# Performance work log

Hardware: AMD Instinct MI355X
Metric: run time of the kernel (lower is better)

The kernel has to match this reference:

```python
import jax, jax.numpy as jnp
import numpy as np

D_MODEL = 1024
N_HEADS = 16
HEAD_DIM = D_MODEL // N_HEADS


def setup_inputs() -> dict:
    key = jax.random.key(0)
    k1, k2, k3 = jax.random.split(key, 3)
    x = jax.random.normal(k1, (4, 2048, D_MODEL), dtype=jnp.float32)
    # torch Linear(d, 3d, bias=False): y = x @ W.T ; store transposed weight [d, 3d]
    scale = 1.0 / np.sqrt(D_MODEL)
    W_qkv = jax.random.normal(k2, (D_MODEL, 3 * D_MODEL), dtype=jnp.float32) * scale
    W_proj = jax.random.normal(k3, (D_MODEL, D_MODEL), dtype=jnp.float32) * scale
    return {"x": x, "W_qkv": W_qkv, "W_proj": W_proj}


def reference(x, W_qkv, W_proj):
    B, T, C = x.shape
    h, d = N_HEADS, HEAD_DIM
    qkv = x @ W_qkv                      # [B,T,3C]
    q, k, v = jnp.split(qkv, 3, axis=-1)
    def split_heads(t):
        return t.reshape(B, T, h, d).transpose(0, 2, 1, 3)  # [B,h,T,d]
    q, k, v = map(split_heads, (q, k, v))
    att = jnp.einsum('bhqd,bhkd->bhqk', q, k) / np.sqrt(d)  # [B,h,T,T]
    causal = jnp.tril(jnp.ones((T, T), dtype=bool))
    att = jnp.where(causal, att, -jnp.inf)
    att = jax.nn.softmax(att, axis=-1)
    # dropout = 0.0 (eval mode): no-op
    y = jnp.einsum('bhqk,bhkd->bhqd', att, v)               # [B,h,T,d]
    y = y.transpose(0, 2, 1, 3).reshape(B, T, C)
    return y @ W_proj
```

## Files before the change

### kernel.cpp

```cpp
#include <hip/hip_runtime.h>

#define T_SEQ 2048
#define D_MODEL 1024
#define NB 4
#define NH 16
#define HD 64

typedef __attribute__((ext_vector_type(8))) __bf16 bf16x8;
typedef __attribute__((ext_vector_type(4))) __bf16 bf16x4;
typedef __attribute__((ext_vector_type(4))) float f32x4;

__device__ __forceinline__ void gload_lds16(const void* g, void* l) {
  __builtin_amdgcn_global_load_lds((const __attribute__((address_space(1))) unsigned int*)g,
                                   (__attribute__((address_space(3))) unsigned int*)l,
                                   16, 0, 0);
}

__device__ __forceinline__ unsigned int pack_bf16_2(float e0, float e1) {
  unsigned short u0 = __builtin_bit_cast(unsigned short, (__bf16)e0);
  unsigned short u1 = __builtin_bit_cast(unsigned short, (__bf16)e1);
  return (unsigned int)u0 | ((unsigned int)u1 << 16);
}

__global__ __launch_bounds__(256) void cvt_bf16_kernel(const float* __restrict__ s,
                                                       __bf16* __restrict__ d, int n) {
  int i = (blockIdx.x * 256 + threadIdx.x) * 8;
  if (i >= n) return;
  float4 a = *(const float4*)(s + i);
  float4 b = *(const float4*)(s + i + 4);
  bf16x8 v;
  v[0] = (__bf16)a.x; v[1] = (__bf16)a.y; v[2] = (__bf16)a.z; v[3] = (__bf16)a.w;
  v[4] = (__bf16)b.x; v[5] = (__bf16)b.y; v[6] = (__bf16)b.z; v[7] = (__bf16)b.w;
  *(bf16x8*)(d + i) = v;
}

__global__ __launch_bounds__(256) void transpose_cvt_kernel(const float* __restrict__ W,
                                                            __bf16* __restrict__ Wt,
                                                            int K, int N) {
  __shared__ float t[32][33];
  int tx = threadIdx.x, ty = threadIdx.y;
  int n0 = blockIdx.x * 32, k0 = blockIdx.y * 32;
#pragma unroll
  for (int r = 0; r < 4; ++r)
    t[ty + r * 8][tx] = W[(size_t)(k0 + ty + r * 8) * N + n0 + tx];
  __syncthreads();
#pragma unroll
  for (int r = 0; r < 4; ++r)
    Wt[(size_t)(n0 + ty + r * 8) * K + k0 + tx] = (__bf16)t[tx][ty + r * 8];
}

__global__ __launch_bounds__(256) void extract_vt_kernel(const __bf16* __restrict__ qkv,
                                                         __bf16* __restrict__ Vt) {
  __shared__ __bf16 t[32][34];
  int tx = threadIdx.x, ty = threadIdx.y;
  int tt = blockIdx.x * 32;
  int dt = blockIdx.y * 32;
  int bh = blockIdx.z;
  int b = bh >> 4, h = bh & 15;
#pragma unroll
  for (int r = 0; r < 4; ++r)
    t[ty + r * 8][tx] = qkv[(size_t)(b * T_SEQ + tt + ty + r * 8) * 3072 + 2048 + h * HD + dt + tx];
  __syncthreads();
#pragma unroll
  for (int r = 0; r < 4; ++r)
    Vt[(size_t)(bh * HD + dt + ty + r * 8) * T_SEQ + tt + tx] = t[tx][ty + r * 8];
}

template <typename OutT>
__global__ __launch_bounds__(256) void gemm_bt(const __bf16* __restrict__ A,
                                               const __bf16* __restrict__ Bt,
                                               OutT* __restrict__ C,
                                               int M, int N, int K) {
  __shared__ __bf16 lA[128 * 64];
  __shared__ __bf16 lB[128 * 64];
  int tid = threadIdx.x;
  int lane = tid & 63, w = tid >> 6;
  int wm = w >> 1, wn = w & 1;
  int nwgx = gridDim.x;
  int lid = blockIdx.y * nwgx + blockIdx.x;
  int cpx = (nwgx * gridDim.y) >> 3;
  int swz = (lid & 7) * cpx + (lid >> 3);
  int bn = swz % nwgx, bm = swz / nwgx;
  f32x4 acc[4][4] = {};
  for (int kt = 0; kt < K; kt += 64) {
#pragma unroll
    for (int it = 0; it < 4; ++it) {
      int o = it * 4096 + tid * 16;
      int row = o >> 7;
      int ss = ((o >> 4) & 7) ^ (row & 7);
      gload_lds16(A + (size_t)(bm * 128 + row) * K + kt + ss * 8, (char*)lA + o);
      gload_lds16(Bt + (size_t)(bn * 128 + row) * K + kt + ss * 8, (char*)lB + o);
    }
    __syncthreads();
    bf16x8 af[4][2], bfv[4][2];
#pragma unroll
    for (int i = 0; i < 4; ++i)
#pragma unroll
      for (int kk = 0; kk < 2; ++kk) {
        int ra = wm * 64 + i * 16 + (lane & 15);
        int sa = ((lane >> 4) + kk * 4) ^ (ra & 7);
        af[i][kk] = *(const bf16x8*)((const char*)lA + ra * 128 + sa * 16);
        int rb = wn * 64 + i * 16 + (lane & 15);
        int sb = ((lane >> 4) + kk * 4) ^ (rb & 7);
        bfv[i][kk] = *(const bf16x8*)((const char*)lB + rb * 128 + sb * 16);
      }
#pragma unroll
    for (int kk = 0; kk < 2; ++kk)
#pragma unroll
      for (int i = 0; i < 4; ++i)
#pragma unroll
        for (int j = 0; j < 4; ++j)
          acc[i][j] = __builtin_amdgcn_mfma_f32_16x16x32_bf16(af[i][kk], bfv[j][kk], acc[i][j], 0, 0, 0);
    __syncthreads();
  }
#pragma unroll
  for (int i = 0; i < 4; ++i)
#pragma unroll
    for (int j = 0; j < 4; ++j)
#pragma unroll
      for (int r = 0; r < 4; ++r) {
        int row = bm * 128 + wm * 64 + i * 16 + (lane >> 4) * 4 + r;
        int col = bn * 128 + wn * 64 + j * 16 + (lane & 15);
        C[(size_t)row * N + col] = (OutT)acc[i][j][r];
      }
}

__global__ __launch_bounds__(128) void attn_kernel(const __bf16* __restrict__ qkv,
                                                   const __bf16* __restrict__ Vt,
                                                   __bf16* __restrict__ Y) {
  __shared__ __bf16 lK[2][64 * 64];
  __shared__ __bf16 lV[2][64 * 64];
  int tid = threadIdx.x, lane = tid & 63, w = tid >> 6;
  int q = lane & 15, g = lane >> 4;

  int l = blockIdx.x;
  int pairHB = ((l & 7) << 3) | (l >> 7);
  int p = (l >> 3) & 15;
  int h = pairHB & 15, b = pairHB >> 4;

  const float SCALE = 0.125f * 1.44269504088896f;
  const f32x4 fzero = {0.f, 0.f, 0.f, 0.f};

#pragma unroll 1
  for (int pass = 0; pass < 2; ++pass) {
    int qt = pass ? p : 31 - p;

    bf16x8 qf[2][2];
#pragma unroll
    for (int qi = 0; qi < 2; ++qi) {
      const __bf16* qp =
          qkv + (size_t)(b * T_SEQ + qt * 64 + w * 32 + qi * 16 + q) * 3072 + h * HD;
      qf[qi][0] = *(const bf16x8*)(qp + g * 8);
      qf[qi][1] = *(const bf16x8*)(qp + 32 + g * 8);
#pragma unroll
      for (int kk = 0; kk < 2; ++kk)
#pragma unroll
        for (int jj = 0; jj < 8; ++jj)
          qf[qi][kk][jj] = (__bf16)((float)qf[qi][kk][jj] * SCALE);
    }

    float m[2] = {-INFINITY, -INFINITY}, lsum[2] = {0.f, 0.f};
    f32x4 yacc[2][4];
#pragma unroll
    for (int qi = 0; qi < 2; ++qi)
#pragma unroll
      for (int f = 0; f < 4; ++f) yacc[qi][f] = fzero;

    asm volatile("s_waitcnt vmcnt(0)" ::: "memory");
    __builtin_amdgcn_sched_barrier(0);

    auto STAGE = [&](int kvt, int bi) {
#pragma unroll
      for (int it = 0; it < 4; ++it) {
        int o = it * 2048 + tid * 16;
        int row = o >> 7;
        int ss = ((o >> 4) & 7) ^ (row & 7);
        gload_lds16(qkv + (size_t)(b * T_SEQ + kvt * 64 + row) * 3072 + 1024 + h * HD + ss * 8,
                    (char*)lK[bi] + o);
        gload_lds16(Vt + (size_t)((b * NH + h) * HD + row) * T_SEQ + kvt * 64 + ss * 8,
                    (char*)lV[bi] + o);
      }
    };

    STAGE(0, 0);

#pragma unroll 1
    for (int kvt = 0; kvt <= qt; ++kvt) {
      int cur = kvt & 1;
      if (kvt < qt) {
        STAGE(kvt + 1, cur ^ 1);
        asm volatile("s_waitcnt vmcnt(8)" ::: "memory");
      } else {
        asm volatile("s_waitcnt vmcnt(0)" ::: "memory");
      }
      __builtin_amdgcn_sched_barrier(0);
      __builtin_amdgcn_s_barrier();
      __builtin_amdgcn_sched_barrier(0);

      f32x4 s[2][4];
#pragma unroll
      for (int qi = 0; qi < 2; ++qi)
#pragma unroll
        for (int f = 0; f < 4; ++f) s[qi][f] = fzero;
      const char* Kbase = (const char*)lK[cur];
      __builtin_amdgcn_s_setprio(1);
#pragma unroll
      for (int kk = 0; kk < 2; ++kk)
#pragma unroll
        for (int f = 0; f < 4; ++f) {
          int rk = f * 16 + q;
          int sk = (g + kk * 4) ^ (rk & 7);
          bf16x8 kf = *(const bf16x8*)(Kbase + rk * 128 + sk * 16);
#pragma unroll
          for (int qi = 0; qi < 2; ++qi)
            s[qi][f] = __builtin_amdgcn_mfma_f32_16x16x32_bf16(kf, qf[qi][kk], s[qi][f], 0, 0, 0);
        }
      __builtin_amdgcn_s_setprio(0);

      if (kvt == qt) {
#pragma unroll
        for (int qi = 0; qi < 2; ++qi) {
          int qloc = w * 32 + qi * 16 + q;
#pragma unroll
          for (int f = 0; f < 4; ++f)
#pragma unroll
            for (int r = 0; r < 4; ++r)
              if (f * 16 + g * 4 + r > qloc) s[qi][f][r] = -INFINITY;
        }
      }

      float mx[2];
#pragma unroll
      for (int qi = 0; qi < 2; ++qi) {
        float v = fmaxf(fmaxf(fmaxf(s[qi][0][0], s[qi][0][1]), fmaxf(s[qi][0][2], s[qi][0][3])),
                        fmaxf(fmaxf(s[qi][1][0], s[qi][1][1]), fmaxf(s[qi][1][2], s[qi][1][3])));
        v = fmaxf(v, fmaxf(fmaxf(fmaxf(s[qi][2][0], s[qi][2][1]), fmaxf(s[qi][2][2], s[qi][2][3])),
                           fmaxf(fmaxf(s[qi][3][0], s[qi][3][1]), fmaxf(s[qi][3][2], s[qi][3][3]))));
        v = fmaxf(v, __shfl_xor(v, 16, 64));
        v = fmaxf(v, __shfl_xor(v, 32, 64));
        mx[qi] = v;
      }

      float growth = fmaxf(mx[0] - m[0], mx[1] - m[1]);
      if (__any(growth > 8.0f)) {
#pragma unroll
        for (int qi = 0; qi < 2; ++qi) {
          float mn = fmaxf(m[qi], mx[qi]);
          float al = exp2f(m[qi] - mn);
          m[qi] = mn;
          lsum[qi] *= al;
#pragma unroll
          for (int r = 0; r < 4; ++r) {
            float ar = __shfl(al, g * 4 + r, 64);
#pragma unroll
            for (int f = 0; f < 4; ++f) yacc[qi][f][r] *= ar;
          }
        }
      }

      unsigned int Wd[2][4][2];
#pragma unroll
      for (int qi = 0; qi < 2; ++qi) {
        float ps = 0.f;
#pragma unroll
        for (int f = 0; f < 4; ++f)
#pragma unroll
          for (int hh = 0; hh < 2; ++hh) {
            float e0 = exp2f(s[qi][f][2 * hh] - m[qi]);
            float e1 = exp2f(s[qi][f][2 * hh + 1] - m[qi]);
            ps += e0 + e1;
            Wd[qi][f][hh] = pack_bf16_2(e0, e1);
          }
        lsum[qi] += ps;
      }

      int srcA = ((g & 1) << 5) | q;
      int srcB = srcA + 16;
      bool hisel = (g >= 2);
      bf16x8 pa[2][2];
#pragma unroll
      for (int qi = 0; qi < 2; ++qi)
#pragma unroll
        for (int kk = 0; kk < 2; ++kk) {
          unsigned int pw[4];
#pragma unroll
          for (int t = 0; t < 4; ++t) {
            int src = (t < 2) ? srcA : srcB;
            unsigned int c0 = (unsigned int)__shfl((int)Wd[qi][2 * kk][t & 1], src, 64);
            unsigned int c1 = (unsigned int)__shfl((int)Wd[qi][2 * kk + 1][t & 1], src, 64);
            pw[t] = hisel ? c1 : c0;
          }
          uint4 u = make_uint4(pw[0], pw[1], pw[2], pw[3]);
          pa[qi][kk] = __builtin_bit_cast(bf16x8, u);
        }

      const char* Vbase = (const char*)lV[cur];
      __builtin_amdgcn_s_setprio(1);
#pragma unroll
      for (int kk = 0; kk < 2; ++kk)
#pragma unroll
        for (int f = 0; f < 4; ++f) {
          int rv = f * 16 + q;
          int sv2 = (g + kk * 4) ^ (rv & 7);
          bf16x8 vf = *(const bf16x8*)(Vbase + rv * 128 + sv2 * 16);
#pragma unroll
          for (int qi = 0; qi < 2; ++qi)
            yacc[qi][f] = __builtin_amdgcn_mfma_f32_16x16x32_bf16(pa[qi][kk], vf, yacc[qi][f], 0, 0, 0);
        }
      __builtin_amdgcn_s_setprio(0);

      __builtin_amdgcn_sched_barrier(0);
      asm volatile("s_waitcnt lgkmcnt(0)" ::: "memory");
      __builtin_amdgcn_s_barrier();
      __builtin_amdgcn_sched_barrier(0);
    }

#pragma unroll
    for (int qi = 0; qi < 2; ++qi) {
      float ls = lsum[qi];
      ls += __shfl_xor(ls, 16, 64);
      ls += __shfl_xor(ls, 32, 64);
      float linv = 1.0f / ls;
      int qrow = qt * 64 + w * 32 + qi * 16 + g * 4;
#pragma unroll
      for (int r = 0; r < 4; ++r) {
        float lr = __shfl(linv, g * 4 + r, 64);
#pragma unroll
        for (int f = 0; f < 4; ++f) {
          Y[(size_t)(b * T_SEQ + qrow + r) * D_MODEL + h * HD + f * 16 + q] =
              (__bf16)(yacc[qi][f][r] * lr);
        }
      }
    }
  }
}

extern "C" void kernel_launch(void* const* d_in, const int* in_sizes, int n_in,
                              void* d_out, int out_size, void* d_ws, size_t ws_size,
                              hipStream_t stream) {
  const float* x = (const float*)d_in[0];
  const float* Wqkv = (const float*)d_in[1];
  const float* Wproj = (const float*)d_in[2];
  float* out = (float*)d_out;
  char* ws = (char*)d_ws;

  __bf16* Xbf     = (__bf16*)(ws);
  __bf16* Wqkv_t  = (__bf16*)(ws + 16777216);
  __bf16* Wproj_t = (__bf16*)(ws + 23068672);
  __bf16* QKV     = (__bf16*)(ws + 25165824);
  __bf16* Vt      = (__bf16*)(ws + 75497472);
  __bf16* Yb      = (__bf16*)(ws + 92274688);

  cvt_bf16_kernel<<<4096, 256, 0, stream>>>(x, Xbf, NB * T_SEQ * D_MODEL);
  transpose_cvt_kernel<<<dim3(96, 32), dim3(32, 8), 0, stream>>>(Wqkv, Wqkv_t, 1024, 3072);
  transpose_cvt_kernel<<<dim3(32, 32), dim3(32, 8), 0, stream>>>(Wproj, Wproj_t, 1024, 1024);
  gemm_bt<__bf16><<<dim3(24, 64), 256, 0, stream>>>(Xbf, Wqkv_t, QKV, 8192, 3072, 1024);
  extract_vt_kernel<<<dim3(64, 2, 64), dim3(32, 8), 0, stream>>>(QKV, Vt);
  attn_kernel<<<1024, 128, 0, stream>>>(QKV, Vt, Yb);
  gemm_bt<float><<<dim3(8, 64), 256, 0, stream>>>(Yb, Wproj_t, out, 8192, 1024, 1024);
}
```

Baseline: 299.7 us.

## Split attention into one q-tile per block and drop K/V double buffering

Each attention block now handles a single 64-row query tile instead of a balanced pair of tiles, doubling the grid to 2048 blocks ordered longest-first. The double-buffered K/V LDS staging with explicit vmcnt waits is replaced by a single buffer loaded then synchronised each iteration, halving LDS use and adding a launch_bounds occupancy hint. The aim is more resident blocks per CU to hide load latency through occupancy, at the cost of losing in-block prefetch overlap and the paired load balancing.

```diff
diff --git a/kernel.cpp b/kernel.cpp
--- a/kernel.cpp
+++ b/kernel.cpp
@@ -125,211 +125,189 @@
       }
 }
 
-__global__ __launch_bounds__(128) void attn_kernel(const __bf16* __restrict__ qkv,
-                                                   const __bf16* __restrict__ Vt,
-                                                   __bf16* __restrict__ Y) {
-  __shared__ __bf16 lK[2][64 * 64];
-  __shared__ __bf16 lV[2][64 * 64];
+__global__ __launch_bounds__(128, 4) void attn_kernel(const __bf16* __restrict__ qkv,
+                                                      const __bf16* __restrict__ Vt,
+                                                      __bf16* __restrict__ Y) {
+  __shared__ __bf16 lK[64 * 64];
+  __shared__ __bf16 lV[64 * 64];
   int tid = threadIdx.x, lane = tid & 63, w = tid >> 6;
   int q = lane & 15, g = lane >> 4;
 
   int l = blockIdx.x;
-  int pairHB = ((l & 7) << 3) | (l >> 7);
-  int p = (l >> 3) & 15;
+  int x = l & 7;
+  int i = l >> 3;
+  int hbLocal = i & 7;
+  int qt = 31 - (i >> 3);
+  int pairHB = x * 8 + hbLocal;
   int h = pairHB & 15, b = pairHB >> 4;
 
   const float SCALE = 0.125f * 1.44269504088896f;
   const f32x4 fzero = {0.f, 0.f, 0.f, 0.f};
 
+  bf16x8 qf[2][2];
+#pragma unroll
+  for (int qi = 0; qi < 2; ++qi) {
+    const __bf16* qp =
+        qkv + (size_t)(b * T_SEQ + qt * 64 + w * 32 + qi * 16 + q) * 3072 + h * HD;
+    qf[qi][0] = *(const bf16x8*)(qp + g * 8);
+    qf[qi][1] = *(const bf16x8*)(qp + 32 + g * 8);
+#pragma unroll
+    for (int kk = 0; kk < 2; ++kk)
+#pragma unroll
+      for (int jj = 0; jj < 8; ++jj)
+        qf[qi][kk][jj] = (__bf16)((float)qf[qi][kk][jj] * SCALE);
+  }
+
+  float m[2] = {-INFINITY, -INFINITY}, lsum[2] = {0.f, 0.f};
+  f32x4 yacc[2][4];
+#pragma unroll
+  for (int qi = 0; qi < 2; ++qi)
+#pragma unroll
+    for (int f = 0; f < 4; ++f) yacc[qi][f] = fzero;
+
 #pragma unroll 1
-  for (int pass = 0; pass < 2; ++pass) {
-    int qt = pass ? p : 31 - p;
-
-    bf16x8 qf[2][2];
+  for (int kvt = 0; kvt <= qt; ++kvt) {
+#pragma unroll
+    for (int it = 0; it < 4; ++it) {
+      int o = it * 2048 + tid * 16;
+      int row = o >> 7;
+      int ss = ((o >> 4) & 7) ^ (row & 7);
+      gload_lds16(qkv + (size_t)(b * T_SEQ + kvt * 64 + row) * 3072 + 1024 + h * HD + ss * 8,
+                  (char*)lK + o);
+      gload_lds16(Vt + (size_t)((b * NH + h) * HD + row) * T_SEQ + kvt * 64 + ss * 8,
+                  (char*)lV + o);
+    }
+    __syncthreads();
+
+    f32x4 s[2][4];
+#pragma unroll
+    for (int qi = 0; qi < 2; ++qi)
+#pragma unroll
+      for (int f = 0; f < 4; ++f) s[qi][f] = fzero;
+    const char* Kbase = (const char*)lK;
+    __builtin_amdgcn_s_setprio(1);
+#pragma unroll
+    for (int kk = 0; kk < 2; ++kk)
+#pragma unroll
+      for (int f = 0; f < 4; ++f) {
+        int rk = f * 16 + q;
+        int sk = (g + kk * 4) ^ (rk & 7);
+        bf16x8 kf = *(const bf16x8*)(Kbase + rk * 128 + sk * 16);
+#pragma unroll
+        for (int qi = 0; qi < 2; ++qi)
+          s[qi][f] = __builtin_amdgcn_mfma_f32_16x16x32_bf16(kf, qf[qi][kk], s[qi][f], 0, 0, 0);
+      }
+    __builtin_amdgcn_s_setprio(0);
+
+    if (kvt == qt) {
+#pragma unroll
+      for (int qi = 0; qi < 2; ++qi) {
+        int qloc = w * 32 + qi * 16 + q;
+#pragma unroll
+        for (int f = 0; f < 4; ++f)
+#pragma unroll
+          for (int r = 0; r < 4; ++r)
+            if (f * 16 + g * 4 + r > qloc) s[qi][f][r] = -INFINITY;
+      }
+    }
+
+    float mx[2];
 #pragma unroll
     for (int qi = 0; qi < 2; ++qi) {
-      const __bf16* qp =
-          qkv + (size_t)(b * T_SEQ + qt * 64 + w * 32 + qi * 16 + q) * 3072 + h * HD;
-      qf[qi][0] = *(const bf16x8*)(qp + g * 8);
-      qf[qi][1] = *(const bf16x8*)(qp + 32 + g * 8);
-#pragma unroll
-      for (int kk = 0; kk < 2; ++kk)
-#pragma unroll
-        for (int jj = 0; jj < 8; ++jj)
-          qf[qi][kk][jj] = (__bf16)((float)qf[qi][kk][jj] * SCALE);
-    }
-
-    float m[2] = {-INFINITY, -INFINITY}, lsum[2] = {0.f, 0.f};
-    f32x4 yacc[2][4];
+      float v = fmaxf(fmaxf(fmaxf(s[qi][0][0], s[qi][0][1]), fmaxf(s[qi][0][2], s[qi][0][3])),
+                      fmaxf(fmaxf(s[qi][1][0], s[qi][1][1]), fmaxf(s[qi][1][2], s[qi][1][3])));
+      v = fmaxf(v, fmaxf(fmaxf(fmaxf(s[qi][2][0], s[qi][2][1]), fmaxf(s[qi][2][2], s[qi][2][3])),
+                         fmaxf(fmaxf(s[qi][3][0], s[qi][3][1]), fmaxf(s[qi][3][2], s[qi][3][3]))));
+      v = fmaxf(v, __shfl_xor(v, 16, 64));
+      v = fmaxf(v, __shfl_xor(v, 32, 64));
+      mx[qi] = v;
+    }
+
+    float growth = fmaxf(mx[0] - m[0], mx[1] - m[1]);
+    if (__any(growth > 8.0f)) {
+#pragma unroll
+      for (int qi = 0; qi < 2; ++qi) {
+        float mn = fmaxf(m[qi], mx[qi]);
+        float al = exp2f(m[qi] - mn);
+        m[qi] = mn;
+        lsum[qi] *= al;
+#pragma unroll
+        for (int r = 0; r < 4; ++r) {
+          float ar = __shfl(al, g * 4 + r, 64);
+#pragma unroll
+          for (int f = 0; f < 4; ++f) yacc[qi][f][r] *= ar;
+        }
+      }
+    }
+
+    unsigned int Wd[2][4][2];
+#pragma unroll
+    for (int qi = 0; qi < 2; ++qi) {
+      float ps = 0.f;
+#pragma unroll
+      for (int f = 0; f < 4; ++f)
+#pragma unroll
+        for (int hh = 0; hh < 2; ++hh) {
+          float e0 = exp2f(s[qi][f][2 * hh] - m[qi]);
+          float e1 = exp2f(s[qi][f][2 * hh + 1] - m[qi]);
+          ps += e0 + e1;
+          Wd[qi][f][hh] = pack_bf16_2(e0, e1);
+        }
+      lsum[qi] += ps;
+    }
+
+    int srcA = ((g & 1) << 5) | q;
+    int srcB = srcA + 16;
+    bool hisel = (g >= 2);
+    bf16x8 pa[2][2];
 #pragma unroll
     for (int qi = 0; qi < 2; ++qi)
 #pragma unroll
-      for (int f = 0; f < 4; ++f) yacc[qi][f] = fzero;
-
-    asm volatile("s_waitcnt vmcnt(0)" ::: "memory");
-    __builtin_amdgcn_sched_barrier(0);
-
-    auto STAGE = [&](int kvt, int bi) {
-#pragma unroll
-      for (int it = 0; it < 4; ++it) {
-        int o = it * 2048 + tid * 16;
-        int row = o >> 7;
-        int ss = ((o >> 4) & 7) ^ (row & 7);
-        gload_lds16(qkv + (size_t)(b * T_SEQ + kvt * 64 + row) * 3072 + 1024 + h * HD + ss * 8,
-                    (char*)lK[bi] + o);
-        gload_lds16(Vt + (size_t)((b * NH + h) * HD + row) * T_SEQ + kvt * 64 + ss * 8,
-                    (char*)lV[bi] + o);
-      }
-    };
-
-    STAGE(0, 0);
-
-#pragma unroll 1
-    for (int kvt = 0; kvt <= qt; ++kvt) {
-      int cur = kvt & 1;
-      if (kvt < qt) {
-        STAGE(kvt + 1, cur ^ 1);
-        asm volatile("s_waitcnt vmcnt(8)" ::: "memory");
-      } else {
-        asm volatile("s_waitcnt vmcnt(0)" ::: "memory");
-      }
-      __builtin_amdgcn_sched_barrier(0);
-      __builtin_amdgcn_s_barrier();
-      __builtin_amdgcn_sched_barrier(0);
-
-      f32x4 s[2][4];
-#pragma unroll
-      for (int qi = 0; qi < 2; ++qi)
-#pragma unroll
-        for (int f = 0; f < 4; ++f) s[qi][f] = fzero;
-      const char* Kbase = (const char*)lK[cur];
-      __builtin_amdgcn_s_setprio(1);
-#pragma unroll
-      for (int kk = 0; kk < 2; ++kk)
-#pragma unroll
-        for (int f = 0; f < 4; ++f) {
-          int rk = f * 16 + q;
-          int sk = (g + kk * 4) ^ (rk & 7);
-          bf16x8 kf = *(const bf16x8*)(Kbase + rk * 128 + sk * 16);
-#pragma unroll
-          for (int qi = 0; qi < 2; ++qi)
-            s[qi][f] = __builtin_amdgcn_mfma_f32_16x16x32_bf16(kf, qf[qi][kk], s[qi][f], 0, 0, 0);
+      for (int kk = 0; kk < 2; ++kk) {
+        unsigned int pw[4];
+#pragma unroll
+        for (int t = 0; t < 4; ++t) {
+          int src = (t < 2) ? srcA : srcB;
+          unsigned int c0 = (unsigned int)__shfl((int)Wd[qi][2 * kk][t & 1], src, 64);
+          unsigned int c1 = (unsigned int)__shfl((int)Wd[qi][2 * kk + 1][t & 1], src, 64);
+          pw[t] = hisel ? c1 : c0;
         }
-      __builtin_amdgcn_s_setprio(0);
-
-      if (kvt == qt) {
-#pragma unroll
-        for (int qi = 0; qi < 2; ++qi) {
-          int qloc = w * 32 + qi * 16 + q;
-#pragma unroll
-          for (int f = 0; f < 4; ++f)
-#pragma unroll
-            for (int r = 0; r < 4; ++r)
-              if (f * 16 + g * 4 + r > qloc) s[qi][f][r] = -INFINITY;
-        }
-      }
-
-      float mx[2];
-#pragma unroll
-      for (int qi = 0; qi < 2; ++qi) {
-        float v = fmaxf(fmaxf(fmaxf(s[qi][0][0], s[qi][0][1]), fmaxf(s[qi][0][2], s[qi][0][3])),
-                        fmaxf(fmaxf(s[qi][1][0], s[qi][1][1]), fmaxf(s[qi][1][2], s[qi][1][3])));
-        v = fmaxf(v, fmaxf(fmaxf(fmaxf(s[qi][2][0], s[qi][2][1]), fmaxf(s[qi][2][2], s[qi][2][3])),
-                           fmaxf(fmaxf(s[qi][3][0], s[qi][3][1]), fmaxf(s[qi][3][2], s[qi][3][3]))));
-        v = fmaxf(v, __shfl_xor(v, 16, 64));
-        v = fmaxf(v, __shfl_xor(v, 32, 64));
-        mx[qi] = v;
-      }
-
-      float growth = fmaxf(mx[0] - m[0], mx[1] - m[1]);
-      if (__any(growth > 8.0f)) {
-#pragma unroll
-        for (int qi = 0; qi < 2; ++qi) {
-          float mn = fmaxf(m[qi], mx[qi]);
-          float al = exp2f(m[qi] - mn);
-          m[qi] = mn;
-          lsum[qi] *= al;
-#pragma unroll
-          for (int r = 0; r < 4; ++r) {
-            float ar = __shfl(al, g * 4 + r, 64);
-#pragma unroll
-            for (int f = 0; f < 4; ++f) yacc[qi][f][r] *= ar;
-          }
-        }
-      }
-
-      unsigned int Wd[2][4][2];
-#pragma unroll
-      for (int qi = 0; qi < 2; ++qi) {
-        float ps = 0.f;
-#pragma unroll
-        for (int f = 0; f < 4; ++f)
-#pragma unroll
-          for (int hh = 0; hh < 2; ++hh) {
-            float e0 = exp2f(s[qi][f][2 * hh] - m[qi]);
-            float e1 = exp2f(s[qi][f][2 * hh + 1] - m[qi]);
-            ps += e0 + e1;
-            Wd[qi][f][hh] = pack_bf16_2(e0, e1);
-          }
-        lsum[qi] += ps;
-      }
-
-      int srcA = ((g & 1) << 5) | q;
-      int srcB = srcA + 16;
-      bool hisel = (g >= 2);
-      bf16x8 pa[2][2];
-#pragma unroll
-      for (int qi = 0; qi < 2; ++qi)
-#pragma unroll
-        for (int kk = 0; kk < 2; ++kk) {
-          unsigned int pw[4];
-#pragma unroll
-          for (int t = 0; t < 4; ++t) {
-            int src = (t < 2) ? srcA : srcB;
-            unsigned int c0 = (unsigned int)__shfl((int)Wd[qi][2 * kk][t & 1], src, 64);
-            unsigned int c1 = (unsigned int)__shfl((int)Wd[qi][2 * kk + 1][t & 1], src, 64);
-            pw[t] = hisel ? c1 : c0;
-          }
-          uint4 u = make_uint4(pw[0], pw[1], pw[2], pw[3]);
-          pa[qi][kk] = __builtin_bit_cast(bf16x8, u);
-        }
-
-      const char* Vbase = (const char*)lV[cur];
-      __builtin_amdgcn_s_setprio(1);
-#pragma unroll
-      for (int kk = 0; kk < 2; ++kk)
-#pragma unroll
-        for (int f = 0; f < 4; ++f) {
-          int rv = f * 16 + q;
-          int sv2 = (g + kk * 4) ^ (rv & 7);
-          bf16x8 vf = *(const bf16x8*)(Vbase + rv * 128 + sv2 * 16);
-#pragma unroll
-          for (int qi = 0; qi < 2; ++qi)
-            yacc[qi][f] = __builtin_amdgcn_mfma_f32_16x16x32_bf16(pa[qi][kk], vf, yacc[qi][f], 0, 0, 0);
-        }
-      __builtin_amdgcn_s_setprio(0);
-
-      __builtin_amdgcn_sched_barrier(0);
-      asm volatile("s_waitcnt lgkmcnt(0)" ::: "memory");
-      __builtin_amdgcn_s_barrier();
-      __builtin_amdgcn_sched_barrier(0);
-    }
-
-#pragma unroll
-    for (int qi = 0; qi < 2; ++qi) {
-      float ls = lsum[qi];
-      ls += __shfl_xor(ls, 16, 64);
-      ls += __shfl_xor(ls, 32, 64);
-      float linv = 1.0f / ls;
-      int qrow = qt * 64 + w * 32 + qi * 16 + g * 4;
-#pragma unroll
-      for (int r = 0; r < 4; ++r) {
-        float lr = __shfl(linv, g * 4 + r, 64);
-#pragma unroll
-        for (int f = 0; f < 4; ++f) {
-          Y[(size_t)(b * T_SEQ + qrow + r) * D_MODEL + h * HD + f * 16 + q] =
-              (__bf16)(yacc[qi][f][r] * lr);
-        }
+        uint4 u = make_uint4(pw[0], pw[1], pw[2], pw[3]);
+        pa[qi][kk] = __builtin_bit_cast(bf16x8, u);
+      }
+
+    const char* Vbase = (const char*)lV;
+    __builtin_amdgcn_s_setprio(1);
+#pragma unroll
+    for (int kk = 0; kk < 2; ++kk)
+#pragma unroll
+      for (int f = 0; f < 4; ++f) {
+        int rv = f * 16 + q;
+        int sv2 = (g + kk * 4) ^ (rv & 7);
+        bf16x8 vf = *(const bf16x8*)(Vbase + rv * 128 + sv2 * 16);
+#pragma unroll
+        for (int qi = 0; qi < 2; ++qi)
+          yacc[qi][f] = __builtin_amdgcn_mfma_f32_16x16x32_bf16(pa[qi][kk], vf, yacc[qi][f], 0, 0, 0);
+      }
+    __builtin_amdgcn_s_setprio(0);
+
+    __syncthreads();
+  }
+
+#pragma unroll
+  for (int qi = 0; qi < 2; ++qi) {
+    float ls = lsum[qi];
+    ls += __shfl_xor(ls, 16, 64);
+    ls += __shfl_xor(ls, 32, 64);
+    float linv = 1.0f / ls;
+    int qrow = qt * 64 + w * 32 + qi * 16 + g * 4;
+#pragma unroll
+    for (int r = 0; r < 4; ++r) {
+      float lr = __shfl(linv, g * 4 + r, 64);
+#pragma unroll
+      for (int f = 0; f < 4; ++f) {
+        Y[(size_t)(b * T_SEQ + qrow + r) * D_MODEL + h * HD + f * 16 + q] =
+            (__bf16)(yacc[qi][f][r] * lr);
       }
     }
   }
@@ -356,6 +334,6 @@
   transpose_cvt_kernel<<<dim3(32, 32), dim3(32, 8), 0, stream>>>(Wproj, Wproj_t, 1024, 1024);
   gemm_bt<__bf16><<<dim3(24, 64), 256, 0, stream>>>(Xbf, Wqkv_t, QKV, 8192, 3072, 1024);
   extract_vt_kernel<<<dim3(64, 2, 64), dim3(32, 8), 0, stream>>>(QKV, Vt);
-  attn_kernel<<<1024, 128, 0, stream>>>(QKV, Vt, Yb);
+  attn_kernel<<<2048, 128, 0, stream>>>(QKV, Vt, Yb);
   gemm_bt<float><<<dim3(8, 64), 256, 0, stream>>>(Yb, Wproj_t, out, 8192, 1024, 1024);
 }
```

New measurement: 318.9 us. 1.06x slower.
